# Kernel optimization log

Hardware: AMD Instinct MI355X
Metric: run time of the kernel (lower is better)

Reference implementation:

```python
import jax, jax.numpy as jnp
import numpy as np

CUTOFF = 5.0
P = 6               # envelope polynomial power
NUM_RBF = 6
NUM_SBF = 7
EMBED = 128
TYPE_EMBED = 64
OUT_EMBED = 256
INT_EMBED = 64      # angle_int_embed_size
BASIS_EMBED = 8
N_BLOCKS = 4
N_DENSE_OUT = 3
N_RES_BEFORE = 1
N_RES_AFTER = 2
N_SPECIES = 16
NUM_TARGETS = 1
N_ATOMS = 4096
N_EDGES = 65536
N_TRIPLETS = 524288

# first 6 positive roots of spherical Bessel j_l, l = 0..6
BESSEL_ZEROS = np.array([
    [3.141593, 6.283185, 9.424778, 12.566371, 15.707963, 18.849556],
    [4.493409, 7.725252, 10.904122, 14.066194, 17.220755, 20.371303],
    [5.763459, 9.095011, 12.322941, 15.514603, 18.689036, 21.853874],
    [6.987932, 10.417119, 13.698023, 16.923621, 20.121806, 23.304247],
    [8.182561, 11.704907, 15.039665, 18.301256, 21.525418, 24.727566],
    [9.355812, 12.966530, 16.354710, 19.653152, 22.904551, 26.126750],
    [10.512835, 14.207392, 17.647975, 20.983463, 24.262768, 27.507868]], dtype=np.float32)

act = jax.nn.silu  # swish


def envelope(x):
    a = -(P + 1) * (P + 2) / 2.0
    b = float(P * (P + 2))
    c = -P * (P + 1) / 2.0
    env = 1.0 / x + a * x ** (P - 1) + b * x ** P + c * x ** (P + 1)
    return jnp.where(x < 1.0, env, 0.0)


def radial_bessel(d):
    # d: (E,) -> (E, NUM_RBF)
    x = d / CUTOFF
    n = jnp.arange(1, NUM_RBF + 1, dtype=jnp.float32)
    return np.float32(np.sqrt(2.0 / CUTOFF)) * envelope(x)[:, None] * jnp.sin(jnp.pi * n[None, :] * x[:, None])


def spherical_basis(d_kj, angles, triplet_mask):
    # d_kj: (T,), angles: (T,) -> (T, NUM_SBF * NUM_RBF)
    x = jnp.maximum(d_kj / CUTOFF, 1e-6)
    env = envelope(x)
    zeros = jnp.asarray(BESSEL_ZEROS)
    radial = []
    for l in range(NUM_SBF):
        a = zeros[l][None, :] * x[:, None]           # (T, NUM_RBF)
        j0 = jnp.sin(a) / a
        if l == 0:
            radial.append(j0)
            continue
        j1 = jnp.sin(a) / a ** 2 - jnp.cos(a) / a
        jm2, jm1 = j0, j1
        for ll in range(2, l + 1):
            jm2, jm1 = jm1, (2 * ll - 1) / a * jm1 - jm2
        radial.append(jm1)
    radial = jnp.stack(radial, axis=1)               # (T, NUM_SBF, NUM_RBF)
    ct = jnp.cos(angles)
    Pl = [jnp.ones_like(ct), ct]
    for l in range(2, NUM_SBF):
        Pl.append(((2 * l - 1) * ct * Pl[l - 1] - (l - 1) * Pl[l - 2]) / l)
    sph = jnp.stack([np.float32(np.sqrt((2 * l + 1) / (4.0 * np.pi))) * Pl[l] for l in range(NUM_SBF)], axis=1)  # (T, NUM_SBF)
    sbf = (env[:, None, None] * radial * sph[:, :, None]).reshape(-1, NUM_SBF * NUM_RBF)
    return jnp.where(triplet_mask[:, None], sbf, 0.0)


def _forward(distances, angles, species_embed, emb_rbf_w, emb_rbf_b, emb_dense_w, emb_dense_b,
             out_rbf_w, out_up_w, out_dense_w, out_dense_b, out_final_w,
             int_ji_w, int_ji_b, int_kj_w, int_kj_b, int_rbf1_w, int_rbf2_w, int_down_w,
             int_sbf1_w, int_sbf2_w, int_up_w, int_res1_w, int_res1_b, int_skip_w, int_skip_b,
             int_res2_w, int_res2_b,
             species, idx_i, idx_j, reduce_to_ji, expand_to_kj, edge_mask, triplet_mask):
    n_particles = species.shape[0]
    n_edges = distances.shape[0]
    d = jnp.where(edge_mask, distances, 2.0 * CUTOFF)       # masked edges -> env = 0
    rbf = radial_bessel(d)                                  # (E, 6)
    sbf = spherical_basis(d[expand_to_kj], angles, triplet_mask)  # (T, 42)

    # embedding block
    h = species_embed[species]                              # (N, 64)
    rbf_emb = rbf @ emb_rbf_w + emb_rbf_b                   # (E, 128)
    m = act(jnp.concatenate([h[idx_j], h[idx_i], rbf_emb], axis=-1) @ emb_dense_w + emb_dense_b)

    def output_block(i, msg):
        atom = jax.ops.segment_sum((rbf @ out_rbf_w[i]) * msg, idx_i, num_segments=n_particles)
        atom = atom @ out_up_w[i]
        for k in range(N_DENSE_OUT):
            atom = act(atom @ out_dense_w[i, k] + out_dense_b[i, k])
        return atom @ out_final_w[i]

    out = output_block(0, m)
    for i in range(N_BLOCKS):
        x_ji = act(m @ int_ji_w[i] + int_ji_b[i])
        x_kj = act(m @ int_kj_w[i] + int_kj_b[i])
        x_kj = x_kj * ((rbf @ int_rbf1_w[i]) @ int_rbf2_w[i])
        x_kj = act(x_kj @ int_down_w[i])                    # (E, 64)
        x_kj = x_kj[expand_to_kj] * ((sbf @ int_sbf1_w[i]) @ int_sbf2_w[i])  # (T, 64)
        x_kj = jax.ops.segment_sum(x_kj, reduce_to_ji, num_segments=n_edges)
        x_kj = act(x_kj @ int_up_w[i])
        hm = x_ji + x_kj
        for r in range(N_RES_BEFORE):
            hm = hm + act(act(hm @ int_res1_w[i, r, 0] + int_res1_b[i, r, 0]) @ int_res1_w[i, r, 1] + int_res1_b[i, r, 1])
        m = act(hm @ int_skip_w[i] + int_skip_b[i]) + m
        for r in range(N_RES_AFTER):
            m = m + act(act(m @ int_res2_w[i, r, 0] + int_res2_b[i, r, 0]) @ int_res2_w[i, r, 1] + int_res2_b[i, r, 1])
        out = out + output_block(i + 1, m)
    return out


def setup_inputs() -> dict:
    key = jax.random.key(0)
    ks = iter(jax.random.split(key, 40))
    def nrm(shape, fan_in):
        return jax.random.normal(next(ks), shape, dtype=jnp.float32) / np.float32(np.sqrt(fan_in))
    inp = {}
    inp['distances'] = 0.5 + 4.45 * jax.random.uniform(next(ks), (N_EDGES,), dtype=jnp.float32)
    inp['angles'] = jnp.pi * jax.random.uniform(next(ks), (N_TRIPLETS,), dtype=jnp.float32)
    inp['species_embed'] = jax.random.normal(next(ks), (N_SPECIES, TYPE_EMBED), dtype=jnp.float32)
    inp['emb_rbf_w'] = nrm((NUM_RBF, EMBED), NUM_RBF)
    inp['emb_rbf_b'] = jnp.zeros((EMBED,), jnp.float32)
    inp['emb_dense_w'] = nrm((2 * TYPE_EMBED + EMBED, EMBED), 2 * TYPE_EMBED + EMBED)
    inp['emb_dense_b'] = jnp.zeros((EMBED,), jnp.float32)
    nb1 = N_BLOCKS + 1
    inp['out_rbf_w'] = nrm((nb1, NUM_RBF, EMBED), NUM_RBF)
    inp['out_up_w'] = nrm((nb1, EMBED, OUT_EMBED), EMBED)
    inp['out_dense_w'] = nrm((nb1, N_DENSE_OUT, OUT_EMBED, OUT_EMBED), OUT_EMBED)
    inp['out_dense_b'] = jnp.zeros((nb1, N_DENSE_OUT, OUT_EMBED), jnp.float32)
    inp['out_final_w'] = nrm((nb1, OUT_EMBED, NUM_TARGETS), OUT_EMBED)
    inp['int_ji_w'] = nrm((N_BLOCKS, EMBED, EMBED), EMBED)
    inp['int_ji_b'] = jnp.zeros((N_BLOCKS, EMBED), jnp.float32)
    inp['int_kj_w'] = nrm((N_BLOCKS, EMBED, EMBED), EMBED)
    inp['int_kj_b'] = jnp.zeros((N_BLOCKS, EMBED), jnp.float32)
    inp['int_rbf1_w'] = nrm((N_BLOCKS, NUM_RBF, BASIS_EMBED), NUM_RBF)
    inp['int_rbf2_w'] = nrm((N_BLOCKS, BASIS_EMBED, EMBED), BASIS_EMBED)
    inp['int_down_w'] = nrm((N_BLOCKS, EMBED, INT_EMBED), EMBED)
    inp['int_sbf1_w'] = nrm((N_BLOCKS, NUM_SBF * NUM_RBF, BASIS_EMBED), NUM_SBF * NUM_RBF)
    inp['int_sbf2_w'] = nrm((N_BLOCKS, BASIS_EMBED, INT_EMBED), BASIS_EMBED)
    inp['int_up_w'] = nrm((N_BLOCKS, INT_EMBED, EMBED), INT_EMBED)
    inp['int_res1_w'] = nrm((N_BLOCKS, N_RES_BEFORE, 2, EMBED, EMBED), EMBED)
    inp['int_res1_b'] = jnp.zeros((N_BLOCKS, N_RES_BEFORE, 2, EMBED), jnp.float32)
    inp['int_skip_w'] = nrm((N_BLOCKS, EMBED, EMBED), EMBED)
    inp['int_skip_b'] = jnp.zeros((N_BLOCKS, EMBED), jnp.float32)
    inp['int_res2_w'] = nrm((N_BLOCKS, N_RES_AFTER, 2, EMBED, EMBED), EMBED)
    inp['int_res2_b'] = jnp.zeros((N_BLOCKS, N_RES_AFTER, 2, EMBED), jnp.float32)
    inp['species'] = jax.random.randint(next(ks), (N_ATOMS,), 0, N_SPECIES)
    inp['idx_i'] = jax.random.randint(next(ks), (N_EDGES,), 0, N_ATOMS)
    inp['idx_j'] = jax.random.randint(next(ks), (N_EDGES,), 0, N_ATOMS)
    inp['reduce_to_ji'] = jax.random.randint(next(ks), (N_TRIPLETS,), 0, N_EDGES)
    inp['expand_to_kj'] = jax.random.randint(next(ks), (N_TRIPLETS,), 0, N_EDGES)
    inp['edge_mask'] = jnp.ones((N_EDGES,), dtype=bool)
    inp['triplet_mask'] = jnp.ones((N_TRIPLETS,), dtype=bool)
    return inp


def reference(distances, angles, species_embed, emb_rbf_w, emb_rbf_b, emb_dense_w, emb_dense_b,
              out_rbf_w, out_up_w, out_dense_w, out_dense_b, out_final_w,
              int_ji_w, int_ji_b, int_kj_w, int_kj_b, int_rbf1_w, int_rbf2_w, int_down_w,
              int_sbf1_w, int_sbf2_w, int_up_w, int_res1_w, int_res1_b, int_skip_w, int_skip_b,
              int_res2_w, int_res2_b,
              species, idx_i, idx_j, reduce_to_ji, expand_to_kj, edge_mask, triplet_mask):
    return _forward(distances, angles, species_embed, emb_rbf_w, emb_rbf_b, emb_dense_w, emb_dense_b,
                    out_rbf_w, out_up_w, out_dense_w, out_dense_b, out_final_w,
                    int_ji_w, int_ji_b, int_kj_w, int_kj_b, int_rbf1_w, int_rbf2_w, int_down_w,
                    int_sbf1_w, int_sbf2_w, int_up_w, int_res1_w, int_res1_b, int_skip_w, int_skip_b,
                    int_res2_w, int_res2_b,
                    species, idx_i, idx_j, reduce_to_ji, expand_to_kj, edge_mask, triplet_mask)
```

## Files before the change

### kernel.cpp

```cpp
#include <hip/hip_runtime.h>
#include <cmath>

typedef __attribute__((ext_vector_type(8))) short bfrag;
typedef __attribute__((ext_vector_type(4))) float f32x4;

__device__ __forceinline__ float silu_f(float x) {
    return x / (1.0f + __expf(-x));
}
__device__ __forceinline__ unsigned short f2bf(float f) {
    unsigned u = __float_as_uint(f);
    unsigned r = (u + 0x7fff + ((u >> 16) & 1)) >> 16;
    return (unsigned short)r;
}
__device__ __forceinline__ float bf2f(unsigned short h) {
    return __uint_as_float(((unsigned)h) << 16);
}
__device__ __forceinline__ unsigned packbf2(float lo, float hi) {
    return ((unsigned)f2bf(hi) << 16) | (unsigned)f2bf(lo);
}
__device__ __forceinline__ short4 hi4f(float a, float b, float c, float d) {
    short4 h;
    h.x = (short)f2bf(a); h.y = (short)f2bf(b);
    h.z = (short)f2bf(c); h.w = (short)f2bf(d);
    return h;
}

template <int KSTEPS, int S, int NS, int ST>
__device__ __forceinline__ void mfma_stage_T(
    const unsigned short* Xs,
    const unsigned short* __restrict__ Whi, const unsigned short* __restrict__ Wlo,
    int Kdim, int arow0, int bcol0, int r16, int kg, f32x4 (&acc)[S][NS]) {
    #pragma unroll
    for (int s = 0; s < S; s++)
        #pragma unroll
        for (int ns = 0; ns < NS; ns++) acc[s][ns] = (f32x4)0.f;
    #pragma unroll
    for (int ks = 0; ks < KSTEPS; ks++) {
        int k0 = ks * 32;
        bfrag wh[NS], wl[NS];
        #pragma unroll
        for (int ns = 0; ns < NS; ns++) {
            size_t o = (size_t)(bcol0 + ns * 16 + r16) * Kdim + k0 + kg * 8;
            wh[ns] = *(const bfrag*)&Whi[o];
            wl[ns] = *(const bfrag*)&Wlo[o];
        }
        #pragma unroll
        for (int s = 0; s < S; s++) {
// ... 2 lines not shown
            for (int ns = 0; ns < NS; ns++) {
                acc[s][ns] = __builtin_amdgcn_mfma_f32_16x16x32_bf16(wh[ns], xh, acc[s][ns], 0, 0, 0);
                acc[s][ns] = __builtin_amdgcn_mfma_f32_16x16x32_bf16(wl[ns], xh, acc[s][ns], 0, 0, 0);
            }
        }
    }
}

__global__ __launch_bounds__(256) void rbf_kernel(const float* __restrict__ d,
                                                  float* __restrict__ rbf, int E) {
    int e = blockIdx.x * 256 + threadIdx.x;
    if (e >= E) return;
    float x = d[e] * 0.2f;
    float env = 0.0f;
    if (x < 1.0f) {
        float x2 = x * x;
        float x5 = x2 * x2 * x;
        env = 1.0f / x + x5 * (-28.0f + x * (48.0f - 21.0f * x));
    }
    const float SQ = 0.63245553f;
    float px = 3.14159265358979f * x;
    #pragma unroll
    for (int n = 1; n <= 6; n++) {
        rbf[e * 6 + n - 1] = SQ * env * sinf(px * (float)n);
    }
}

__global__ __launch_bounds__(128) void embed_pre_kernel(
    const float* __restrict__ se, const float* __restrict__ erw,
    const float* __restrict__ erb, const float* __restrict__ edw,
    float* __restrict__ HWj, float* __restrict__ HWi,
    float* __restrict__ W3, float* __restrict__ b3) {
    int c = threadIdx.x;
    for (int s = 0; s < 16; s++) {
        float aj = 0.f, ai = 0.f;
        for (int k = 0; k < 64; k++) {
            float h = se[s * 64 + k];
            aj += h * edw[k * 128 + c];
            ai += h * edw[(64 + k) * 128 + c];
        }
        HWj[s * 128 + c] = aj;
        HWi[s * 128 + c] = ai;
    }
    for (int r = 0; r < 6; r++) {
        float a = 0.f;
        for (int k = 0; k < 128; k++) a += erw[r * 128 + k] * edw[(128 + k) * 128 + c];
        W3[r * 128 + c] = a;
// ... 29 lines not shown
    int tid = threadIdx.x;
    int r = tid >> 3, cg = tid & 7;
    float4 v = *(const float4*)&Wb[(size_t)(k0 + r) * N + n0 + cg * 4];
    t[r][cg * 4 + 0] = v.x;
    t[r][cg * 4 + 1] = v.y;
    t[r][cg * 4 + 2] = v.z;
    t[r][cg * 4 + 3] = v.w;
    __syncthreads();
    int nl = tid >> 3, kg = tid & 7;
    short4 h4, l4;
    float f0 = t[kg * 4 + 0][nl], f1 = t[kg * 4 + 1][nl];
    float f2 = t[kg * 4 + 2][nl], f3 = t[kg * 4 + 3][nl];
    unsigned short h;
    h = f2bf(f0); h4.x = (short)h; l4.x = (short)f2bf(f0 - bf2f(h));
    h = f2bf(f1); h4.y = (short)h; l4.y = (short)f2bf(f1 - bf2f(h));
    h = f2bf(f2); h4.z = (short)h; l4.z = (short)f2bf(f2 - bf2f(h));
    h = f2bf(f3); h4.w = (short)h; l4.w = (short)f2bf(f3 - bf2f(h));
    size_t o = ((size_t)b * N + n0 + nl) * K + k0 + kg * 4;
    *(short4*)&hi[o] = h4;
    *(short4*)&lo[o] = l4;
}

template <int ACT, int BIAS, int RES>
__global__ __launch_bounds__(512, 2) void mfma_gemmT(
    const float* __restrict__ X, const unsigned short* __restrict__ Whi,
    const unsigned short* __restrict__ Wlo,
    const float* __restrict__ bias, const float* __restrict__ resid,
    float* __restrict__ Y, int M, int K, int N) {
    __shared__ unsigned short Xs[128 * 40];
    int tid = threadIdx.x;
    int bm = blockIdx.x * 128, bn = blockIdx.y * 128;
    int wid = tid >> 6, lane = tid & 63;
    int wr = wid >> 2, wc = wid & 3;
    int r16 = lane & 15, kg = lane >> 4;
    int arow0 = wr * 64, bcol0 = wc * 32;

    f32x4 acc[4][2];
    #pragma unroll
    for (int s = 0; s < 4; s++)
        #pragma unroll
        for (int ns = 0; ns < 2; ns++) acc[s][ns] = (f32x4)0.f;

    for (int k0 = 0; k0 < K; k0 += 32) {
        #pragma unroll
        for (int p = 0; p < 2; p++) {
            int idx = tid + p * 512;
            int row = idx >> 3, cg = idx & 7;
            float4 v = *(const float4*)&X[(size_t)(bm + row) * K + k0 + cg * 4];
            *(short4*)&Xs[row * 40 + cg * 4] = hi4f(v.x, v.y, v.z, v.w);
        }
        __syncthreads();
        bfrag wh[2], wl[2];
        #pragma unroll
        for (int ns = 0; ns < 2; ns++) {
            size_t o = (size_t)(bn + bcol0 + ns * 16 + r16) * K + k0 + kg * 8;
            wh[ns] = *(const bfrag*)&Whi[o];
            wl[ns] = *(const bfrag*)&Wlo[o];
        }
        #pragma unroll
        for (int s = 0; s < 4; s++) {
            bfrag xh = *(const bfrag*)&Xs[(arow0 + s * 16 + r16) * 40 + kg * 8];
            #pragma unroll
            for (int ns = 0; ns < 2; ns++) {
                acc[s][ns] = __builtin_amdgcn_mfma_f32_16x16x32_bf16(wh[ns], xh, acc[s][ns], 0, 0, 0);
                acc[s][ns] = __builtin_amdgcn_mfma_f32_16x16x32_bf16(wl[ns], xh, acc[s][ns], 0, 0, 0);
            }
        }
        __syncthreads();
    }
    #pragma unroll
    for (int s = 0; s < 4; s++) {
        int mm = bm + arow0 + s * 16 + r16;
        #pragma unroll
        for (int ns = 0; ns < 2; ns++) {
            int n0 = bn + bcol0 + ns * 16 + kg * 4;
            float bv[4] = {0.f, 0.f, 0.f, 0.f};
            if (BIAS) {
                float4 b4 = *(const float4*)&bias[n0];
                bv[0] = b4.x; bv[1] = b4.y; bv[2] = b4.z; bv[3] = b4.w;
            }
            float4 o;
            float* op = (float*)&o;
            #pragma unroll
            for (int r = 0; r < 4; r++) {
                float v = acc[s][ns][r] + bv[r];
                if (ACT) v = silu_f(v);
                op[r] = v;
            }
            if (RES) {
                float4 rv = *(const float4*)&resid[(size_t)mm * N + n0];
                o.x += rv.x; o.y += rv.y; o.z += rv.z; o.w += rv.w;
            }
            *(float4*)&Y[(size_t)mm * N + n0] = o;
        }
    }
}

__global__ __launch_bounds__(512, 2) void downpath_kernel(
    const float* __restrict__ m, const float* __restrict__ rbf,
    const float* __restrict__ rbf1, const float* __restrict__ rbf2,
    const unsigned short* __restrict__ jih, const unsigned short* __restrict__ jil,
    const float* __restrict__ jib,
    const unsigned short* __restrict__ kjh, const unsigned short* __restrict__ kjl,
    const float* __restrict__ kjb,
    const unsigned short* __restrict__ dnh, const unsigned short* __restrict__ dnl,
    float* __restrict__ xji, float* __restrict__ xdown) {
    __shared__ unsigned short Xs[128 * 136];
    __shared__ float G8t[8][128];
    __shared__ float Rs[8][128];
    int tid = threadIdx.x, bm = blockIdx.x * 128;
    int wid = tid >> 6, lane = tid & 63;
    int wr = wid >> 2, wc = wid & 3;
    int r16 = lane & 15, kg = lane >> 4;
    int arow0 = wr * 64, bcol0 = wc * 32;

    #pragma unroll
    for (int p = 0; p < 8; p++) {
        int idx = tid + p * 512, row = idx >> 5, cg = idx & 31;
        float4 v = *(const float4*)&m[(size_t)(bm + row) * 128 + cg * 4];
        *(short4*)&Xs[row * 136 + cg * 4] = hi4f(v.x, v.y, v.z, v.w);
    }
    if (tid < 128) {
        float rv[6];
        #pragma unroll
        for (int k = 0; k < 6; k++) rv[k] = rbf[(size_t)(bm + tid) * 6 + k];
        #pragma unroll
        for (int p = 0; p < 8; p++) {
            float a = 0.f;
            #pragma unroll
            for (int k = 0; k < 6; k++) a += rv[k] * rbf1[k * 8 + p];
            G8t[p][tid] = a;
        }
    }
    for (int i = tid; i < 1024; i += 512) Rs[i >> 7][i & 127] = rbf2[i];
    __syncthreads();

    f32x4 acc[4][2];
    mfma_stage_T<4, 4, 2, 136>(Xs, jih, jil, 128, arow0, bcol0, r16, kg, acc);
    #pragma unroll
    for (int s = 0; s < 4; s++) {
        int mm = bm + arow0 + s * 16 + r16;
        #pragma unroll
        for (int ns = 0; ns < 2; ns++) {
            int n0 = bcol0 + ns * 16 + kg * 4;
            float4 b4 = *(const float4*)&jib[n0];
            float4 o;
            o.x = silu_f(acc[s][ns][0] + b4.x);
            o.y = silu_f(acc[s][ns][1] + b4.y);
            o.z = silu_f(acc[s][ns][2] + b4.z);
            o.w = silu_f(acc[s][ns][3] + b4.w);
            *(float4*)&xji[(size_t)mm * 128 + n0] = o;
        }
    }
    mfma_stage_T<4, 4, 2, 136>(Xs, kjh, kjl, 128, arow0, bcol0, r16, kg, acc);
    f32x4 val[4][2];
    #pragma unroll
    for (int s = 0; s < 4; s++) {
        int mrow = arow0 + s * 16 + r16;
        float g8v[8];
        #pragma unroll
        for (int p = 0; p < 8; p++) g8v[p] = G8t[p][mrow];
        #pragma unroll
        for (int ns = 0; ns < 2; ns++) {
            int n0 = bcol0 + ns * 16 + kg * 4;
            float4 b4 = *(const float4*)&kjb[n0];
            float bb[4] = {b4.x, b4.y, b4.z, b4.w};
            #pragma unroll
            for (int r = 0; r < 4; r++) {
                float g = 0.f;
                #pragma unroll
                for (int p = 0; p < 8; p++) g = fmaf(g8v[p], Rs[p][n0 + r], g);
                val[s][ns][r] = silu_f(acc[s][ns][r] + bb[r]) * g;
            }
        }
    }
    __syncthreads();
    #pragma unroll
    for (int s = 0; s < 4; s++)
        #pragma unroll
        for (int ns = 0; ns < 2; ns++)
            *(short4*)&Xs[(arow0 + s * 16 + r16) * 136 + bcol0 + ns * 16 + kg * 4] =
                hi4f(val[s][ns][0], val[s][ns][1], val[s][ns][2], val[s][ns][3]);
    __syncthreads();
    {
        int wr2 = wid >> 1, wc2 = wid & 1;
        f32x4 a2[2][2];
        mfma_stage_T<4, 2, 2, 136>(Xs, dnh, dnl, 128, wr2 * 32, wc2 * 32, r16, kg, a2);
        #pragma unroll
        for (int s = 0; s < 2; s++) {
            int mm = bm + wr2 * 32 + s * 16 + r16;
            #pragma unroll
            for (int ns = 0; ns < 2; ns++) {
                int n0 = wc2 * 32 + ns * 16 + kg * 4;
                float4 o;
                o.x = silu_f(a2[s][ns][0]);
                o.y = silu_f(a2[s][ns][1]);
                o.z = silu_f(a2[s][ns][2]);
                o.w = silu_f(a2[s][ns][3]);
                *(float4*)&xdown[(size_t)mm * 64 + n0] = o;
            }
        }
    }
}

__global__ __launch_bounds__(512, 2) void chain_kernel(
    const float* __restrict__ seg, const float* __restrict__ xji, float* __restrict__ m,
    const unsigned short* __restrict__ uph, const unsigned short* __restrict__ upl,
    const unsigned short* __restrict__ r1h, const unsigned short* __restrict__ r1l,
    const float* __restrict__ r1b,
    const unsigned short* __restrict__ skh, const unsigned short* __restrict__ skl,
    const float* __restrict__ skb,
    const unsigned short* __restrict__ r2h, const unsigned short* __restrict__ r2l,
    const float* __restrict__ r2b) {
    __shared__ unsigned short Xs[128 * 136];
    int tid = threadIdx.x, bm = blockIdx.x * 128;
    int wid = tid >> 6, lane = tid & 63;
    int wr = wid >> 2, wc = wid & 3;
    int r16 = lane & 15, kg = lane >> 4;
    int arow0 = wr * 64, bcol0 = wc * 32;

    #pragma unroll
    for (int p = 0; p < 4; p++) {
        int idx = tid + p * 512, row = idx >> 4, cg = idx & 15;
        float4 v = *(const float4*)&seg[(size_t)(bm + row) * 64 + cg * 4];
        *(short4*)&Xs[row * 136 + cg * 4] = hi4f(v.x, v.y, v.z, v.w);
    }
    __syncthreads();

    f32x4 acc[4][2], res[4][2];

    mfma_stage_T<2, 4, 2, 136>(Xs, uph, upl, 64, arow0, bcol0, r16, kg, acc);
    #pragma unroll
    for (int s = 0; s < 4; s++) {
        int mm = bm + arow0 + s * 16 + r16;
        #pragma unroll
        for (int ns = 0; ns < 2; ns++) {
            int n0 = bcol0 + ns * 16 + kg * 4;
            float4 xv = *(const float4*)&xji[(size_t)mm * 128 + n0];
            res[s][ns][0] = silu_f(acc[s][ns][0]) + xv.x;
            res[s][ns][1] = silu_f(acc[s][ns][1]) + xv.y;
            res[s][ns][2] = silu_f(acc[s][ns][2]) + xv.z;
            res[s][ns][3] = silu_f(acc[s][ns][3]) + xv.w;
        }
    }
    __syncthreads();
    #pragma unroll
    for (int s = 0; s < 4; s++)
        #pragma unroll
        for (int ns = 0; ns < 2; ns++)
            *(short4*)&Xs[(arow0 + s * 16 + r16) * 136 + bcol0 + ns * 16 + kg * 4] =
                hi4f(res[s][ns][0], res[s][ns][1], res[s][ns][2], res[s][ns][3]);
    __syncthreads();

    mfma_stage_T<4, 4, 2, 136>(Xs, r1h, r1l, 128, arow0, bcol0, r16, kg, acc);
    __syncthreads();
    #pragma unroll
    for (int s = 0; s < 4; s++)
        #pragma unroll
        for (int ns = 0; ns < 2; ns++) {
            int n0 = bcol0 + ns * 16 + kg * 4;
            float4 b4 = *(const float4*)&r1b[n0];
            *(short4*)&Xs[(arow0 + s * 16 + r16) * 136 + n0] =
                hi4f(silu_f(acc[s][ns][0] + b4.x), silu_f(acc[s][ns][1] + b4.y),
                     silu_f(acc[s][ns][2] + b4.z), silu_f(acc[s][ns][3] + b4.w));
        }
    __syncthreads();
    mfma_stage_T<4, 4, 2, 136>(Xs, r1h + 16384, r1l + 16384, 128, arow0, bcol0, r16, kg, acc);
    #pragma unroll
    for (int s = 0; s < 4; s++)
        #pragma unroll
        for (int ns = 0; ns < 2; ns++) {
            int n0 = bcol0 + ns * 16 + kg * 4;
            float4 b4 = *(const float4*)&r1b[128 + n0];
            res[s][ns][0] += silu_f(acc[s][ns][0] + b4.x);
            res[s][ns][1] += silu_f(acc[s][ns][1] + b4.y);
            res[s][ns][2] += silu_f(acc[s][ns][2] + b4.z);
            res[s][ns][3] += silu_f(acc[s][ns][3] + b4.w);
        }
    __syncthreads();
    #pragma unroll
    for (int s = 0; s < 4; s++)
        #pragma unroll
        for (int ns = 0; ns < 2; ns++)
            *(short4*)&Xs[(arow0 + s * 16 + r16) * 136 + bcol0 + ns * 16 + kg * 4] =
                hi4f(res[s][ns][0], res[s][ns][1], res[s][ns][2], res[s][ns][3]);
    __syncthreads();

    mfma_stage_T<4, 4, 2, 136>(Xs, skh, skl, 128, arow0, bcol0, r16, kg, acc);
    #pragma unroll
    for (int s = 0; s < 4; s++) {
        int mm = bm + arow0 + s * 16 + r16;
        #pragma unroll
        for (int ns = 0; ns < 2; ns++) {
            int n0 = bcol0 + ns * 16 + kg * 4;
            float4 b4 = *(const float4*)&skb[n0];
            float4 mv = *(const float4*)&m[(size_t)mm * 128 + n0];
            res[s][ns][0] = silu_f(acc[s][ns][0] + b4.x) + mv.x;
            res[s][ns][1] = silu_f(acc[s][ns][1] + b4.y) + mv.y;
            res[s][ns][2] = silu_f(acc[s][ns][2] + b4.z) + mv.z;
            res[s][ns][3] = silu_f(acc[s][ns][3] + b4.w) + mv.w;
        }
    }
    __syncthreads();
    #pragma unroll
    for (int s = 0; s < 4; s++)
        #pragma unroll
        for (int ns = 0; ns < 2; ns++)
            *(short4*)&Xs[(arow0 + s * 16 + r16) * 136 + bcol0 + ns * 16 + kg * 4] =
                hi4f(res[s][ns][0], res[s][ns][1], res[s][ns][2], res[s][ns][3]);
    __syncthreads();

    #pragma unroll
    for (int rr = 0; rr < 2; rr++) {
        const unsigned short* wh = r2h + (size_t)rr * 2 * 16384;
        const unsigned short* wl = r2l + (size_t)rr * 2 * 16384;
        const float* bb = r2b + (size_t)rr * 2 * 128;
        mfma_stage_T<4, 4, 2, 136>(Xs, wh, wl, 128, arow0, bcol0, r16, kg, acc);
        __syncthreads();
        #pragma unroll
        for (int s = 0; s < 4; s++)
            #pragma unroll
            for (int ns = 0; ns < 2; ns++) {
                int n0 = bcol0 + ns * 16 + kg * 4;
                float4 b4 = *(const float4*)&bb[n0];
                *(short4*)&Xs[(arow0 + s * 16 + r16) * 136 + n0] =
                    hi4f(silu_f(acc[s][ns][0] + b4.x), silu_f(acc[s][ns][1] + b4.y),
                         silu_f(acc[s][ns][2] + b4.z), silu_f(acc[s][ns][3] + b4.w));
            }
        __syncthreads();
        mfma_stage_T<4, 4, 2, 136>(Xs, wh + 16384, wl + 16384, 128, arow0, bcol0, r16, kg, acc);
        #pragma unroll
        for (int s = 0; s < 4; s++)
            #pragma unroll
            for (int ns = 0; ns < 2; ns++) {
                int n0 = bcol0 + ns * 16 + kg * 4;
                float4 b4 = *(const float4*)&bb[128 + n0];
                res[s][ns][0] += silu_f(acc[s][ns][0] + b4.x);
                res[s][ns][1] += silu_f(acc[s][ns][1] + b4.y);
                res[s][ns][2] += silu_f(acc[s][ns][2] + b4.z);
                res[s][ns][3] += silu_f(acc[s][ns][3] + b4.w);
            }
        if (rr == 0) {
            __syncthreads();
            #pragma unroll
            for (int s = 0; s < 4; s++)
                #pragma unroll
                for (int ns = 0; ns < 2; ns++)
                    *(short4*)&Xs[(arow0 + s * 16 + r16) * 136 + bcol0 + ns * 16 + kg * 4] =
                        hi4f(res[s][ns][0], res[s][ns][1], res[s][ns][2], res[s][ns][3]);
            __syncthreads();
        }
    }
    #pragma unroll
    for (int s = 0; s < 4; s++) {
        int mm = bm + arow0 + s * 16 + r16;
        #pragma unroll
        for (int ns = 0; ns < 2; ns++) {
            int n0 = bcol0 + ns * 16 + kg * 4;
            float4 o;
            o.x = res[s][ns][0]; o.y = res[s][ns][1];
            o.z = res[s][ns][2]; o.w = res[s][ns][3];
            *(float4*)&m[(size_t)mm * 128 + n0] = o;
        }
    }
}

__global__ __launch_bounds__(256) void outseg_kernel(
    const float* __restrict__ rbf, const float* __restrict__ orw,
    const float* __restrict__ m, const int* __restrict__ idx_i,
    float* __restrict__ atom) {
    int gid = blockIdx.x * 256 + threadIdx.x;
    int e = gid >> 7, c = gid & 127;
    float s = 0.f;
    #pragma unroll
    for (int k = 0; k < 6; k++) s += rbf[e * 6 + k] * orw[k * 128 + c];
    atomicAdd(&atom[(size_t)idx_i[e] * 128 + c], s * m[gid]);
}

__global__ __launch_bounds__(64) void final_kernel(
    const float* __restrict__ atom, const float* __restrict__ wf,
    float* __restrict__ out) {
    int a = blockIdx.x, l = threadIdx.x;
    float s = 0.f;
    #pragma unroll
    for (int q = 0; q < 4; q++) s += atom[(size_t)a * 256 + q * 64 + l] * wf[q * 64 + l];
    #pragma unroll
    for (int off = 32; off; off >>= 1) s += __shfl_down(s, off, 64);
    if (l == 0) out[a] += s;
}

__global__ __launch_bounds__(256) void hist_kernel(const int* __restrict__ rji,
                                                   int* __restrict__ hist) {
    int t = blockIdx.x * 256 + threadIdx.x;
    atomicAdd(&hist[rji[t]], 1);
}

__global__ __launch_bounds__(256) void scan1_kernel(const int* __restrict__ hist,
                                                    int* __restrict__ bsum) {
    __shared__ int s[256];
    int i = threadIdx.x;
    s[i] = hist[blockIdx.x * 256 + i];
    __syncthreads();
    for (int o = 128; o; o >>= 1) {
        if (i < o) s[i] += s[i + o];
        __syncthreads();
    }
    if (!i) bsum[blockIdx.x] = s[0];
}

__global__ __launch_bounds__(256) void scan2_kernel(const int* __restrict__ bsum,
                                                    int* __restrict__ boff) {
// ... 41 lines not shown
    perm[pos] = t;
    ekjs[pos] = ekj[t];
}

__global__ __launch_bounds__(256) void sbf_pre_kernel(
    const float* __restrict__ dist, const float* __restrict__ angles,
    const int* __restrict__ perm, const int* __restrict__ ekjs,
    const float* __restrict__ sbf1_all, unsigned short* __restrict__ t32, int T) {
    __shared__ float s1[1344];
    int tid = threadIdx.x;
    for (int i = tid; i < 1344; i += 256) s1[i] = sbf1_all[i];
    __syncthreads();

    int pos = blockIdx.x * 256 + tid;
    int t = perm[pos];
    int e = ekjs[pos];
    float x = fmaxf(dist[e] * 0.2f, 1e-6f);
    float env = 0.f;
    if (x < 1.0f) {
        float x2 = x * x;
        float x5 = x2 * x2 * x;
        env = 1.0f / x + x5 * (-28.0f + x * (48.0f - 21.0f * x));
    }
    float ct = cosf(angles[t]);
    float Pl[7];
    Pl[0] = 1.f;
    Pl[1] = ct;
    #pragma unroll
    for (int l = 2; l < 7; l++)
        Pl[l] = ((2.f * l - 1.f) * ct * Pl[l - 1] - (l - 1.f) * Pl[l - 2]) / (float)l;
    const float sphc[7] = {0.28209479f, 0.48860251f, 0.63078313f, 0.74635267f,
                           0.84628438f, 0.93560257f, 1.01710723f};
    const float BZ[7][6] = {
        {3.141593f, 6.283185f, 9.424778f, 12.566371f, 15.707963f, 18.849556f},
        {4.493409f, 7.725252f, 10.904122f, 14.066194f, 17.220755f, 20.371303f},
        {5.763459f, 9.095011f, 12.322941f, 15.514603f, 18.689036f, 21.853874f},
        {6.987932f, 10.417119f, 13.698023f, 16.923621f, 20.121806f, 23.304247f},
        {8.182561f, 11.704907f, 15.039665f, 18.301256f, 21.525418f, 24.727566f},
        {9.355812f, 12.966530f, 16.354710f, 19.653152f, 22.904551f, 26.126750f},
        {10.512835f, 14.207392f, 17.647975f, 20.983463f, 24.262768f, 27.507868f}};
    float sbf[42];
    #pragma unroll
    for (int l = 0; l < 7; l++) {
        float coef = env * sphc[l] * Pl[l];
        #pragma unroll
        for (int n = 0; n < 6; n++) {
            float a = BZ[l][n] * x;
            float sa, ca;
            sincosf(a, &sa, &ca);
            float inv = 1.0f / a;
            float j;
            if (l == 0) {
                j = sa * inv;
            } else {
                float jm2 = sa * inv;
                float jm1 = (sa * inv - ca) * inv;
                #pragma unroll
                for (int ll = 2; ll <= l; ll++) {
                    float jn = (2.f * ll - 1.f) * inv * jm1 - jm2;
                    jm2 = jm1;
                    jm1 = jn;
                }
                j = jm1;
            }
            sbf[l * 6 + n] = coef * j;
        }
    }
    float acc[32];
    #pragma unroll
    for (int q = 0; q < 32; q++) acc[q] = 0.f;
    #pragma unroll
    for (int k = 0; k < 42; k++) {
        float sv = sbf[k];
// ... 138 lines not shown
    sbf_pre_kernel<<<T / 256, 256, 0, stream>>>(distances, angles, perm, ekjs,
                                                int_sbf1_w, t32, T);

    wconv_kernel<<<dim3(4, 4, 4), 256, 0, stream>>>(int_ji_w, ji_h, ji_l, 128, 128);
    wconv_kernel<<<dim3(4, 4, 4), 256, 0, stream>>>(int_kj_w, kj_h, kj_l, 128, 128);
    wconv_kernel<<<dim3(2, 4, 4), 256, 0, stream>>>(int_down_w, dn_h, dn_l, 128, 64);
    wconv_kernel<<<dim3(4, 2, 4), 256, 0, stream>>>(int_up_w, up_h, up_l, 64, 128);
    wconv_kernel<<<dim3(4, 4, 8), 256, 0, stream>>>(int_res1_w, r1_h, r1_l, 128, 128);
    wconv_kernel<<<dim3(4, 4, 4), 256, 0, stream>>>(int_skip_w, sk_h, sk_l, 128, 128);
    wconv_kernel<<<dim3(4, 4, 16), 256, 0, stream>>>(int_res2_w, r2_h, r2_l, 128, 128);
    wconv_kernel<<<dim3(8, 4, 5), 256, 0, stream>>>(out_up_w, ou_h, ou_l, 128, 256);
    wconv_kernel<<<dim3(8, 8, 15), 256, 0, stream>>>(out_dense_w, od_h, od_l, 256, 256);

    rbf_kernel<<<E / 256, 256, 0, stream>>>(distances, rbf, E);
    embed_pre_kernel<<<1, 128, 0, stream>>>(species_emb, emb_rbf_w, emb_rbf_b,
                                            emb_dense_w, HWj, HWi, W3, b3);
    embed_kernel<<<E * 128 / 256, 256, 0, stream>>>(rbf, species, idx_i, idx_j,
                                                    HWj, HWi, W3, b3, emb_dense_b, m);

    auto outblock = [&](int i, const float* msg) {
        hipMemsetAsync(atom1, 0, (size_t)NA * 128 * sizeof(float), stream);
        outseg_kernel<<<E * 128 / 256, 256, 0, stream>>>(
            rbf, out_rbf_w + (size_t)i * 6 * 128, msg, idx_i, atom1);
        mfma_gemmT<0, 0, 0><<<dim3(NA / 128, 2), 512, 0, stream>>>(
            atom1, ou_h + (size_t)i * 32768, ou_l + (size_t)i * 32768,
            nullptr, nullptr, atom2, NA, 128, 256);
        mfma_gemmT<1, 1, 0><<<dim3(NA / 128, 2), 512, 0, stream>>>(
            atom2, od_h + ((size_t)i * 3 + 0) * 65536, od_l + ((size_t)i * 3 + 0) * 65536,
            out_dense_b + ((size_t)i * 3 + 0) * 256, nullptr, atom3, NA, 256, 256);
        mfma_gemmT<1, 1, 0><<<dim3(NA / 128, 2), 512, 0, stream>>>(
            atom3, od_h + ((size_t)i * 3 + 1) * 65536, od_l + ((size_t)i * 3 + 1) * 65536,
            out_dense_b + ((size_t)i * 3 + 1) * 256, nullptr, atom2, NA, 256, 256);
        mfma_gemmT<1, 1, 0><<<dim3(NA / 128, 2), 512, 0, stream>>>(
            atom2, od_h + ((size_t)i * 3 + 2) * 65536, od_l + ((size_t)i * 3 + 2) * 65536,
            out_dense_b + ((size_t)i * 3 + 2) * 256, nullptr, atom3, NA, 256, 256);
        final_kernel<<<NA, 64, 0, stream>>>(atom3, out_final_w + (size_t)i * 256, out);
    };

    outblock(0, m);

    for (int i = 0; i < 4; i++) {
        downpath_kernel<<<E / 128, 512, 0, stream>>>(
            m, rbf, int_rbf1_w + (size_t)i * 48, int_rbf2_w + (size_t)i * 1024,
            ji_h + (size_t)i * 16384, ji_l + (size_t)i * 16384, int_ji_b + (size_t)i * 128,
            kj_h + (size_t)i * 16384, kj_l + (size_t)i * 16384, int_kj_b + (size_t)i * 128,
            dn_h + (size_t)i * 8192, dn_l + (size_t)i * 8192,
            A, D);
        seg_gather_kernel<<<E * 64 / 256, 256, 0, stream>>>(
            t32 + (size_t)i * T * 8, ekjs, rows, D,
            int_sbf2_w + (size_t)i * 8 * 64, seg, E);
        chain_kernel<<<E / 128, 512, 0, stream>>>(
            seg, A, m,
            up_h + (size_t)i * 8192, up_l + (size_t)i * 8192,
            r1_h + (size_t)i * 32768, r1_l + (size_t)i * 32768, int_res1_b + (size_t)i * 256,
            sk_h + (size_t)i * 16384, sk_l + (size_t)i * 16384, int_skip_b + (size_t)i * 128,
            r2_h + (size_t)i * 65536, r2_l + (size_t)i * 65536, int_res2_b + (size_t)i * 512);
        outblock(i + 1, m);
    }
}
```

Measured before the change: 1.646 ms.

## Halve GEMM row tiles, fuse output dense chain, use fast intrinsics

Row tiles in the GEMM, downpath and chain kernels drop from 128 to 64 rows, with launch bounds raised to 4 blocks per CU, to give more blocks and higher occupancy. The three output dense layers and the final projection are fused into one outchain kernel that keeps activations in shared memory and reduces with LDS atomics. This removes several launches and the round trips through global memory. Float-to-bf16 conversion now uses the packed v_cvt_pk_bf16_f32 instruction. sin, cos, sincos and the silu divide are replaced with fast approximate intrinsics, which may lose a little accuracy.

```diff
diff --git a/kernel.cpp b/kernel.cpp
--- a/kernel.cpp
+++ b/kernel.cpp
@@ -5,7 +5,7 @@
 typedef __attribute__((ext_vector_type(4))) float f32x4;
 
 __device__ __forceinline__ float silu_f(float x) {
-    return x / (1.0f + __expf(-x));
+    return x * __builtin_amdgcn_rcpf(1.0f + __expf(-x));
 }
 __device__ __forceinline__ unsigned short f2bf(float f) {
     unsigned u = __float_as_uint(f);
@@ -18,11 +18,13 @@
 __device__ __forceinline__ unsigned packbf2(float lo, float hi) {
     return ((unsigned)f2bf(hi) << 16) | (unsigned)f2bf(lo);
 }
-__device__ __forceinline__ short4 hi4f(float a, float b, float c, float d) {
-    short4 h;
-    h.x = (short)f2bf(a); h.y = (short)f2bf(b);
-    h.z = (short)f2bf(c); h.w = (short)f2bf(d);
-    return h;
+__device__ __forceinline__ unsigned cvtpk2(float a, float b) {
+    unsigned r;
+    asm("v_cvt_pk_bf16_f32 %0, %1, %2" : "=v"(r) : "v"(a), "v"(b));
+    return r;
+}
+__device__ __forceinline__ uint2 pk4(float a, float b, float c, float d) {
+    return make_uint2(cvtpk2(a, b), cvtpk2(c, d));
 }
 
 template <int KSTEPS, int S, int NS, int ST>
@@ -71,7 +73,7 @@
     float px = 3.14159265358979f * x;
     #pragma unroll
     for (int n = 1; n <= 6; n++) {
-        rbf[e * 6 + n - 1] = SQ * env * sinf(px * (float)n);
+        rbf[e * 6 + n - 1] = SQ * env * __sinf(px * (float)n);
     }
 }
 
@@ -147,32 +149,30 @@
 }
 
 template <int ACT, int BIAS, int RES>
-__global__ __launch_bounds__(512, 2) void mfma_gemmT(
+__global__ __launch_bounds__(512, 4) void mfma_gemmT(
     const float* __restrict__ X, const unsigned short* __restrict__ Whi,
     const unsigned short* __restrict__ Wlo,
     const float* __restrict__ bias, const float* __restrict__ resid,
     float* __restrict__ Y, int M, int K, int N) {
-    __shared__ unsigned short Xs[128 * 40];
+    __shared__ unsigned short Xs[64 * 40];
     int tid = threadIdx.x;
-    int bm = blockIdx.x * 128, bn = blockIdx.y * 128;
+    int bm = blockIdx.x * 64, bn = blockIdx.y * 128;
     int wid = tid >> 6, lane = tid & 63;
     int wr = wid >> 2, wc = wid & 3;
     int r16 = lane & 15, kg = lane >> 4;
-    int arow0 = wr * 64, bcol0 = wc * 32;
-
-    f32x4 acc[4][2];
-    #pragma unroll
-    for (int s = 0; s < 4; s++)
+    int arow0 = wr * 32, bcol0 = wc * 32;
+
+    f32x4 acc[2][2];
+    #pragma unroll
+    for (int s = 0; s < 2; s++)
         #pragma unroll
         for (int ns = 0; ns < 2; ns++) acc[s][ns] = (f32x4)0.f;
 
     for (int k0 = 0; k0 < K; k0 += 32) {
-        #pragma unroll
-        for (int p = 0; p < 2; p++) {
-            int idx = tid + p * 512;
-            int row = idx >> 3, cg = idx & 7;
+        {
+            int row = tid >> 3, cg = tid & 7;
             float4 v = *(const float4*)&X[(size_t)(bm + row) * K + k0 + cg * 4];
-            *(short4*)&Xs[row * 40 + cg * 4] = hi4f(v.x, v.y, v.z, v.w);
+            *(uint2*)&Xs[row * 40 + cg * 4] = pk4(v.x, v.y, v.z, v.w);
         }
         __syncthreads();
         bfrag wh[2], wl[2];
@@ -183,7 +183,7 @@
             wl[ns] = *(const bfrag*)&Wlo[o];
         }
         #pragma unroll
-        for (int s = 0; s < 4; s++) {
+        for (int s = 0; s < 2; s++) {
             bfrag xh = *(const bfrag*)&Xs[(arow0 + s * 16 + r16) * 40 + kg * 8];
             #pragma unroll
             for (int ns = 0; ns < 2; ns++) {
@@ -194,7 +194,7 @@
         __syncthreads();
     }
     #pragma unroll
-    for (int s = 0; s < 4; s++) {
+    for (int s = 0; s < 2; s++) {
         int mm = bm + arow0 + s * 16 + r16;
         #pragma unroll
         for (int ns = 0; ns < 2; ns++) {
@@ -221,7 +221,70 @@
     }
 }
 
-__global__ __launch_bounds__(512, 2) void downpath_kernel(
+__global__ __launch_bounds__(512, 4) void outchain_kernel(
+    const float* __restrict__ atom2,
+    const unsigned short* __restrict__ odh, const unsigned short* __restrict__ odl,
+    const float* __restrict__ odb, const float* __restrict__ wf,
+    float* __restrict__ out) {
+    __shared__ unsigned short Xs[64 * 264];
+    __shared__ float rsum[64];
+    int tid = threadIdx.x, bm = blockIdx.x * 64;
+    int wid = tid >> 6, lane = tid & 63;
+    int wr = wid >> 2, wc = wid & 3;
+    int r16 = lane & 15, kg = lane >> 4;
+    int arow0 = wr * 32, bcol0 = wc * 64;
+    if (tid < 64) rsum[tid] = 0.f;
+
+    #pragma unroll
+    for (int p = 0; p < 8; p++) {
+        int idx = tid + p * 512, row = idx >> 6, cg = idx & 63;
+        float4 v = *(const float4*)&atom2[(size_t)(bm + row) * 256 + cg * 4];
+        *(uint2*)&Xs[row * 264 + cg * 4] = pk4(v.x, v.y, v.z, v.w);
+    }
+    __syncthreads();
+
+    f32x4 acc[2][4];
+    #pragma unroll
+    for (int st = 0; st < 3; st++) {
+        mfma_stage_T<8, 2, 4, 264>(Xs, odh + (size_t)st * 65536, odl + (size_t)st * 65536,
+                                   256, arow0, bcol0, r16, kg, acc);
+        const float* bb = odb + st * 256;
+        __syncthreads();
+        if (st < 2) {
+            #pragma unroll
+            for (int s = 0; s < 2; s++)
+                #pragma unroll
+                for (int ns = 0; ns < 4; ns++) {
+                    int n0 = bcol0 + ns * 16 + kg * 4;
+                    float4 b4 = *(const float4*)&bb[n0];
+                    *(uint2*)&Xs[(arow0 + s * 16 + r16) * 264 + n0] =
+                        pk4(silu_f(acc[s][0 + ns][0] + b4.x), silu_f(acc[s][ns][1] + b4.y),
+                            silu_f(acc[s][ns][2] + b4.z), silu_f(acc[s][ns][3] + b4.w));
+                }
+            __syncthreads();
+        } else {
+            #pragma unroll
+            for (int s = 0; s < 2; s++) {
+                float part = 0.f;
+                #pragma unroll
+                for (int ns = 0; ns < 4; ns++) {
+                    int n0 = bcol0 + ns * 16 + kg * 4;
+                    float4 b4 = *(const float4*)&bb[n0];
+                    float4 w4 = *(const float4*)&wf[n0];
+                    part += silu_f(acc[s][ns][0] + b4.x) * w4.x;
+                    part += silu_f(acc[s][ns][1] + b4.y) * w4.y;
+                    part += silu_f(acc[s][ns][2] + b4.z) * w4.z;
+                    part += silu_f(acc[s][ns][3] + b4.w) * w4.w;
+                }
+                atomicAdd(&rsum[arow0 + s * 16 + r16], part);
+            }
+        }
+    }
+    __syncthreads();
+    if (tid < 64) out[bm + tid] += rsum[tid];
+}
+
+__global__ __launch_bounds__(512, 4) void downpath_kernel(
     const float* __restrict__ m, const float* __restrict__ rbf,
     const float* __restrict__ rbf1, const float* __restrict__ rbf2,
     const unsigned short* __restrict__ jih, const unsigned short* __restrict__ jil,
@@ -230,22 +293,22 @@
     const float* __restrict__ kjb,
     const unsigned short* __restrict__ dnh, const unsigned short* __restrict__ dnl,
     float* __restrict__ xji, float* __restrict__ xdown) {
-    __shared__ unsigned short Xs[128 * 136];
-    __shared__ float G8t[8][128];
+    __shared__ unsigned short Xs[64 * 136];
+    __shared__ float G8t[8][64];
     __shared__ float Rs[8][128];
-    int tid = threadIdx.x, bm = blockIdx.x * 128;
+    int tid = threadIdx.x, bm = blockIdx.x * 64;
     int wid = tid >> 6, lane = tid & 63;
     int wr = wid >> 2, wc = wid & 3;
     int r16 = lane & 15, kg = lane >> 4;
-    int arow0 = wr * 64, bcol0 = wc * 32;
-
-    #pragma unroll
-    for (int p = 0; p < 8; p++) {
+    int arow0 = wr * 32, bcol0 = wc * 32;
+
+    #pragma unroll
+    for (int p = 0; p < 4; p++) {
         int idx = tid + p * 512, row = idx >> 5, cg = idx & 31;
         float4 v = *(const float4*)&m[(size_t)(bm + row) * 128 + cg * 4];
-        *(short4*)&Xs[row * 136 + cg * 4] = hi4f(v.x, v.y, v.z, v.w);
-    }
-    if (tid < 128) {
+        *(uint2*)&Xs[row * 136 + cg * 4] = pk4(v.x, v.y, v.z, v.w);
+    }
+    if (tid < 64) {
         float rv[6];
         #pragma unroll
         for (int k = 0; k < 6; k++) rv[k] = rbf[(size_t)(bm + tid) * 6 + k];
@@ -260,10 +323,10 @@
     for (int i = tid; i < 1024; i += 512) Rs[i >> 7][i & 127] = rbf2[i];
     __syncthreads();
 
-    f32x4 acc[4][2];
-    mfma_stage_T<4, 4, 2, 136>(Xs, jih, jil, 128, arow0, bcol0, r16, kg, acc);
-    #pragma unroll
-    for (int s = 0; s < 4; s++) {
+    f32x4 acc[2][2];
+    mfma_stage_T<4, 2, 2, 136>(Xs, jih, jil, 128, arow0, bcol0, r16, kg, acc);
+    #pragma unroll
+    for (int s = 0; s < 2; s++) {
         int mm = bm + arow0 + s * 16 + r16;
         #pragma unroll
         for (int ns = 0; ns < 2; ns++) {
@@ -277,10 +340,10 @@
             *(float4*)&xji[(size_t)mm * 128 + n0] = o;
         }
     }
-    mfma_stage_T<4, 4, 2, 136>(Xs, kjh, kjl, 128, arow0, bcol0, r16, kg, acc);
-    f32x4 val[4][2];
-    #pragma unroll
-    for (int s = 0; s < 4; s++) {
+    mfma_stage_T<4, 2, 2, 136>(Xs, kjh, kjl, 128, arow0, bcol0, r16, kg, acc);
+    f32x4 val[2][2];
+    #pragma unroll
+    for (int s = 0; s < 2; s++) {
         int mrow = arow0 + s * 16 + r16;
         float g8v[8];
         #pragma unroll
@@ -301,34 +364,31 @@
     }
     __syncthreads();
     #pragma unroll
-    for (int s = 0; s < 4; s++)
+    for (int s = 0; s < 2; s++)
         #pragma unroll
         for (int ns = 0; ns < 2; ns++)
-            *(short4*)&Xs[(arow0 + s * 16 + r16) * 136 + bcol0 + ns * 16 + kg * 4] =
-                hi4f(val[s][ns][0], val[s][ns][1], val[s][ns][2], val[s][ns][3]);
+            *(uint2*)&Xs[(arow0 + s * 16 + r16) * 136 + bcol0 + ns * 16 + kg * 4] =
+                pk4(val[s][ns][0], val[s][ns][1], val[s][ns][2], val[s][ns][3]);
     __syncthreads();
     {
-        int wr2 = wid >> 1, wc2 = wid & 1;
-        f32x4 a2[2][2];
-        mfma_stage_T<4, 2, 2, 136>(Xs, dnh, dnl, 128, wr2 * 32, wc2 * 32, r16, kg, a2);
-        #pragma unroll
-        for (int s = 0; s < 2; s++) {
-            int mm = bm + wr2 * 32 + s * 16 + r16;
-            #pragma unroll
-            for (int ns = 0; ns < 2; ns++) {
-                int n0 = wc2 * 32 + ns * 16 + kg * 4;
-                float4 o;
-                o.x = silu_f(a2[s][ns][0]);
-                o.y = silu_f(a2[s][ns][1]);
-                o.z = silu_f(a2[s][ns][2]);
-                o.w = silu_f(a2[s][ns][3]);
-                *(float4*)&xdown[(size_t)mm * 64 + n0] = o;
-            }
-        }
-    }
-}
-
-__global__ __launch_bounds__(512, 2) void chain_kernel(
+        int ar2 = (wid >> 1) * 16, wc2 = wid & 1;
+        f32x4 a2[1][2];
+        mfma_stage_T<4, 1, 2, 136>(Xs, dnh, dnl, 128, ar2, wc2 * 32, r16, kg, a2);
+        int mm = bm + ar2 + r16;
+        #pragma unroll
+        for (int ns = 0; ns < 2; ns++) {
+            int n0 = wc2 * 32 + ns * 16 + kg * 4;
+            float4 o;
+            o.x = silu_f(a2[0][ns][0]);
+            o.y = silu_f(a2[0][ns][1]);
+            o.z = silu_f(a2[0][ns][2]);
+            o.w = silu_f(a2[0][ns][3]);
+            *(float4*)&xdown[(size_t)mm * 64 + n0] = o;
+        }
+    }
+}
+
+__global__ __launch_bounds__(512, 4) void chain_kernel(
     const float* __restrict__ seg, const float* __restrict__ xji, float* __restrict__ m,
     const unsigned short* __restrict__ uph, const unsigned short* __restrict__ upl,
     const unsigned short* __restrict__ r1h, const unsigned short* __restrict__ r1l,
@@ -337,26 +397,26 @@
     const float* __restrict__ skb,
     const unsigned short* __restrict__ r2h, const unsigned short* __restrict__ r2l,
     const float* __restrict__ r2b) {
-    __shared__ unsigned short Xs[128 * 136];
-    int tid = threadIdx.x, bm = blockIdx.x * 128;
+    __shared__ unsigned short Xs[64 * 136];
+    int tid = threadIdx.x, bm = blockIdx.x * 64;
     int wid = tid >> 6, lane = tid & 63;
     int wr = wid >> 2, wc = wid & 3;
     int r16 = lane & 15, kg = lane >> 4;
-    int arow0 = wr * 64, bcol0 = wc * 32;
-
-    #pragma unroll
-    for (int p = 0; p < 4; p++) {
+    int arow0 = wr * 32, bcol0 = wc * 32;
+
+    #pragma unroll
+    for (int p = 0; p < 2; p++) {
         int idx = tid + p * 512, row = idx >> 4, cg = idx & 15;
         float4 v = *(const float4*)&seg[(size_t)(bm + row) * 64 + cg * 4];
-        *(short4*)&Xs[row * 136 + cg * 4] = hi4f(v.x, v.y, v.z, v.w);
-    }
-    __syncthreads();
-
-    f32x4 acc[4][2], res[4][2];
-
-    mfma_stage_T<2, 4, 2, 136>(Xs, uph, upl, 64, arow0, bcol0, r16, kg, acc);
-    #pragma unroll
-    for (int s = 0; s < 4; s++) {
+        *(uint2*)&Xs[row * 136 + cg * 4] = pk4(v.x, v.y, v.z, v.w);
+    }
+    __syncthreads();
+
+    f32x4 acc[2][2], res[2][2];
+
+    mfma_stage_T<2, 2, 2, 136>(Xs, uph, upl, 64, arow0, bcol0, r16, kg, acc);
+    #pragma unroll
+    for (int s = 0; s < 2; s++) {
         int mm = bm + arow0 + s * 16 + r16;
         #pragma unroll
         for (int ns = 0; ns < 2; ns++) {
@@ -370,29 +430,29 @@
     }
     __syncthreads();
     #pragma unroll
-    for (int s = 0; s < 4; s++)
+    for (int s = 0; s < 2; s++)
         #pragma unroll
         for (int ns = 0; ns < 2; ns++)
-            *(short4*)&Xs[(arow0 + s * 16 + r16) * 136 + bcol0 + ns * 16 + kg * 4] =
-                hi4f(res[s][ns][0], res[s][ns][1], res[s][ns][2], res[s][ns][3]);
-    __syncthreads();
-
-    mfma_stage_T<4, 4, 2, 136>(Xs, r1h, r1l, 128, arow0, bcol0, r16, kg, acc);
-    __syncthreads();
-    #pragma unroll
-    for (int s = 0; s < 4; s++)
+            *(uint2*)&Xs[(arow0 + s * 16 + r16) * 136 + bcol0 + ns * 16 + kg * 4] =
+                pk4(res[s][ns][0], res[s][ns][1], res[s][ns][2], res[s][ns][3]);
+    __syncthreads();
+
+    mfma_stage_T<4, 2, 2, 136>(Xs, r1h, r1l, 128, arow0, bcol0, r16, kg, acc);
+    __syncthreads();
+    #pragma unroll
+    for (int s = 0; s < 2; s++)
         #pragma unroll
         for (int ns = 0; ns < 2; ns++) {
             int n0 = bcol0 + ns * 16 + kg * 4;
             float4 b4 = *(const float4*)&r1b[n0];
-            *(short4*)&Xs[(arow0 + s * 16 + r16) * 136 + n0] =
-                hi4f(silu_f(acc[s][ns][0] + b4.x), silu_f(acc[s][ns][1] + b4.y),
-                     silu_f(acc[s][ns][2] + b4.z), silu_f(acc[s][ns][3] + b4.w));
-        }
-    __syncthreads();
-    mfma_stage_T<4, 4, 2, 136>(Xs, r1h + 16384, r1l + 16384, 128, arow0, bcol0, r16, kg, acc);
-    #pragma unroll
-    for (int s = 0; s < 4; s++)
+            *(uint2*)&Xs[(arow0 + s * 16 + r16) * 136 + n0] =
+                pk4(silu_f(acc[s][ns][0] + b4.x), silu_f(acc[s][ns][1] + b4.y),
+                    silu_f(acc[s][ns][2] + b4.z), silu_f(acc[s][ns][3] + b4.w));
+        }
+    __syncthreads();
+    mfma_stage_T<4, 2, 2, 136>(Xs, r1h + 16384, r1l + 16384, 128, arow0, bcol0, r16, kg, acc);
+    #pragma unroll
+    for (int s = 0; s < 2; s++)
         #pragma unroll
         for (int ns = 0; ns < 2; ns++) {
             int n0 = bcol0 + ns * 16 + kg * 4;
@@ -404,16 +464,16 @@
         }
     __syncthreads();
     #pragma unroll
-    for (int s = 0; s < 4; s++)
+    for (int s = 0; s < 2; s++)
         #pragma unroll
         for (int ns = 0; ns < 2; ns++)
-            *(short4*)&Xs[(arow0 + s * 16 + r16) * 136 + bcol0 + ns * 16 + kg * 4] =
-                hi4f(res[s][ns][0], res[s][ns][1], res[s][ns][2], res[s][ns][3]);
-    __syncthreads();
-
-    mfma_stage_T<4, 4, 2, 136>(Xs, skh, skl, 128, arow0, bcol0, r16, kg, acc);
-    #pragma unroll
-    for (int s = 0; s < 4; s++) {
+            *(uint2*)&Xs[(arow0 + s * 16 + r16) * 136 + bcol0 + ns * 16 + kg * 4] =
+                pk4(res[s][ns][0], res[s][ns][1], res[s][ns][2], res[s][ns][3]);
+    __syncthreads();
+
+    mfma_stage_T<4, 2, 2, 136>(Xs, skh, skl, 128, arow0, bcol0, r16, kg, acc);
+    #pragma unroll
+    for (int s = 0; s < 2; s++) {
         int mm = bm + arow0 + s * 16 + r16;
         #pragma unroll
         for (int ns = 0; ns < 2; ns++) {
@@ -428,11 +488,11 @@
     }
     __syncthreads();
     #pragma unroll
-    for (int s = 0; s < 4; s++)
+    for (int s = 0; s < 2; s++)
         #pragma unroll
         for (int ns = 0; ns < 2; ns++)
-            *(short4*)&Xs[(arow0 + s * 16 + r16) * 136 + bcol0 + ns * 16 + kg * 4] =
-                hi4f(res[s][ns][0], res[s][ns][1], res[s][ns][2], res[s][ns][3]);
+            *(uint2*)&Xs[(arow0 + s * 16 + r16) * 136 + bcol0 + ns * 16 + kg * 4] =
+                pk4(res[s][ns][0], res[s][ns][1], res[s][ns][2], res[s][ns][3]);
     __syncthreads();
 
     #pragma unroll
@@ -440,22 +500,22 @@
         const unsigned short* wh = r2h + (size_t)rr * 2 * 16384;
         const unsigned short* wl = r2l + (size_t)rr * 2 * 16384;
         const float* bb = r2b + (size_t)rr * 2 * 128;
-        mfma_stage_T<4, 4, 2, 136>(Xs, wh, wl, 128, arow0, bcol0, r16, kg, acc);
-        __syncthreads();
-        #pragma unroll
-        for (int s = 0; s < 4; s++)
+        mfma_stage_T<4, 2, 2, 136>(Xs, wh, wl, 128, arow0, bcol0, r16, kg, acc);
+        __syncthreads();
+        #pragma unroll
+        for (int s = 0; s < 2; s++)
             #pragma unroll
             for (int ns = 0; ns < 2; ns++) {
                 int n0 = bcol0 + ns * 16 + kg * 4;
                 float4 b4 = *(const float4*)&bb[n0];
-                *(short4*)&Xs[(arow0 + s * 16 + r16) * 136 + n0] =
-                    hi4f(silu_f(acc[s][ns][0] + b4.x), silu_f(acc[s][ns][1] + b4.y),
-                         silu_f(acc[s][ns][2] + b4.z), silu_f(acc[s][ns][3] + b4.w));
-            }
-        __syncthreads();
-        mfma_stage_T<4, 4, 2, 136>(Xs, wh + 16384, wl + 16384, 128, arow0, bcol0, r16, kg, acc);
-        #pragma unroll
-        for (int s = 0; s < 4; s++)
+                *(uint2*)&Xs[(arow0 + s * 16 + r16) * 136 + n0] =
+                    pk4(silu_f(acc[s][ns][0] + b4.x), silu_f(acc[s][ns][1] + b4.y),
+                        silu_f(acc[s][ns][2] + b4.z), silu_f(acc[s][ns][3] + b4.w));
+            }
+        __syncthreads();
+        mfma_stage_T<4, 2, 2, 136>(Xs, wh + 16384, wl + 16384, 128, arow0, bcol0, r16, kg, acc);
+        #pragma unroll
+        for (int s = 0; s < 2; s++)
             #pragma unroll
             for (int ns = 0; ns < 2; ns++) {
                 int n0 = bcol0 + ns * 16 + kg * 4;
@@ -468,16 +528,16 @@
         if (rr == 0) {
             __syncthreads();
             #pragma unroll
-            for (int s = 0; s < 4; s++)
+            for (int s = 0; s < 2; s++)
                 #pragma unroll
                 for (int ns = 0; ns < 2; ns++)
-                    *(short4*)&Xs[(arow0 + s * 16 + r16) * 136 + bcol0 + ns * 16 + kg * 4] =
-                        hi4f(res[s][ns][0], res[s][ns][1], res[s][ns][2], res[s][ns][3]);
+                    *(uint2*)&Xs[(arow0 + s * 16 + r16) * 136 + bcol0 + ns * 16 + kg * 4] =
+                        pk4(res[s][ns][0], res[s][ns][1], res[s][ns][2], res[s][ns][3]);
             __syncthreads();
         }
     }
     #pragma unroll
-    for (int s = 0; s < 4; s++) {
+    for (int s = 0; s < 2; s++) {
         int mm = bm + arow0 + s * 16 + r16;
         #pragma unroll
         for (int ns = 0; ns < 2; ns++) {
@@ -500,18 +560,6 @@
     #pragma unroll
     for (int k = 0; k < 6; k++) s += rbf[e * 6 + k] * orw[k * 128 + c];
     atomicAdd(&atom[(size_t)idx_i[e] * 128 + c], s * m[gid]);
-}
-
-__global__ __launch_bounds__(64) void final_kernel(
-    const float* __restrict__ atom, const float* __restrict__ wf,
-    float* __restrict__ out) {
-    int a = blockIdx.x, l = threadIdx.x;
-    float s = 0.f;
-    #pragma unroll
-    for (int q = 0; q < 4; q++) s += atom[(size_t)a * 256 + q * 64 + l] * wf[q * 64 + l];
-    #pragma unroll
-    for (int off = 32; off; off >>= 1) s += __shfl_down(s, off, 64);
-    if (l == 0) out[a] += s;
 }
 
 __global__ __launch_bounds__(256) void hist_kernel(const int* __restrict__ rji,
@@ -599,7 +647,7 @@
         float x5 = x2 * x2 * x;
         env = 1.0f / x + x5 * (-28.0f + x * (48.0f - 21.0f * x));
     }
-    float ct = cosf(angles[t]);
+    float ct = __cosf(angles[t]);
     float Pl[7];
     Pl[0] = 1.f;
     Pl[1] = ct;
@@ -624,8 +672,8 @@
         for (int n = 0; n < 6; n++) {
             float a = BZ[l][n] * x;
             float sa, ca;
-            sincosf(a, &sa, &ca);
-            float inv = 1.0f / a;
+            __sincosf(a, &sa, &ca);
+            float inv = __builtin_amdgcn_rcpf(a);
             float j;
             if (l == 0) {
                 j = sa * inv;
@@ -810,25 +858,18 @@
         hipMemsetAsync(atom1, 0, (size_t)NA * 128 * sizeof(float), stream);
         outseg_kernel<<<E * 128 / 256, 256, 0, stream>>>(
             rbf, out_rbf_w + (size_t)i * 6 * 128, msg, idx_i, atom1);
-        mfma_gemmT<0, 0, 0><<<dim3(NA / 128, 2), 512, 0, stream>>>(
+        mfma_gemmT<0, 0, 0><<<dim3(NA / 64, 2), 512, 0, stream>>>(
             atom1, ou_h + (size_t)i * 32768, ou_l + (size_t)i * 32768,
             nullptr, nullptr, atom2, NA, 128, 256);
-        mfma_gemmT<1, 1, 0><<<dim3(NA / 128, 2), 512, 0, stream>>>(
-            atom2, od_h + ((size_t)i * 3 + 0) * 65536, od_l + ((size_t)i * 3 + 0) * 65536,
-            out_dense_b + ((size_t)i * 3 + 0) * 256, nullptr, atom3, NA, 256, 256);
-        mfma_gemmT<1, 1, 0><<<dim3(NA / 128, 2), 512, 0, stream>>>(
-            atom3, od_h + ((size_t)i * 3 + 1) * 65536, od_l + ((size_t)i * 3 + 1) * 65536,
-            out_dense_b + ((size_t)i * 3 + 1) * 256, nullptr, atom2, NA, 256, 256);
-        mfma_gemmT<1, 1, 0><<<dim3(NA / 128, 2), 512, 0, stream>>>(
-            atom2, od_h + ((size_t)i * 3 + 2) * 65536, od_l + ((size_t)i * 3 + 2) * 65536,
-            out_dense_b + ((size_t)i * 3 + 2) * 256, nullptr, atom3, NA, 256, 256);
-        final_kernel<<<NA, 64, 0, stream>>>(atom3, out_final_w + (size_t)i * 256, out);
+        outchain_kernel<<<NA / 64, 512, 0, stream>>>(
+            atom2, od_h + (size_t)i * 3 * 65536, od_l + (size_t)i * 3 * 65536,
+            out_dense_b + (size_t)i * 3 * 256, out_final_w + (size_t)i * 256, out);
     };
 
     outblock(0, m);
 
     for (int i = 0; i < 4; i++) {
-        downpath_kernel<<<E / 128, 512, 0, stream>>>(
+        downpath_kernel<<<E / 64, 512, 0, stream>>>(
             m, rbf, int_rbf1_w + (size_t)i * 48, int_rbf2_w + (size_t)i * 1024,
             ji_h + (size_t)i * 16384, ji_l + (size_t)i * 16384, int_ji_b + (size_t)i * 128,
             kj_h + (size_t)i * 16384, kj_l + (size_t)i * 16384, int_kj_b + (size_t)i * 128,
@@ -837,7 +878,7 @@
         seg_gather_kernel<<<E * 64 / 256, 256, 0, stream>>>(
             t32 + (size_t)i * T * 8, ekjs, rows, D,
             int_sbf2_w + (size_t)i * 8 * 64, seg, E);
-        chain_kernel<<<E / 128, 512, 0, stream>>>(
+        chain_kernel<<<E / 64, 512, 0, stream>>>(
             seg, A, m,
             up_h + (size_t)i * 8192, up_l + (size_t)i * 8192,
             r1_h + (size_t)i * 32768, r1_l + (size_t)i * 32768, int_res1_b + (size_t)i * 256,
```

New measurement: 1.742 ms. 1.06x slower.
